# Kernel tuning notes

Hardware: AMD Instinct MI355X
Metric: run time of the kernel (lower is better)

The kernel has to match this reference:

```python
import jax, jax.numpy as jnp
import numpy as np

L, B, N, C = 6, 8, 300, 20
H, W = 28, 28
GT_H, GT_W = 448, 448


def _pair_similarity(rm_b):
    # rm_b: (N, H, W). Pairwise (IoU + Dice)/2 between thresholded (>0.7) masks.
    T = (rm_b.reshape(N, H * W) > 0.7).astype(jnp.float32)
    inter = T @ T.T                                  # (N, N)
    s = T.sum(axis=1)
    union = s[:, None] + s[None, :] - inter
    tot = s[:, None] + s[None, :]
    iou = jnp.where(union == 0, 1.0, inter / jnp.where(union == 0, 1.0, union))
    dice = jnp.where(tot == 0, 1.0, 2.0 * inter / jnp.where(tot == 0, 1.0, tot))
    return 0.5 * (iou + dice)


def _cluster(S_b, cls_sc):
    # NMS-style greedy transitive expansion from the top-scoring candidate.
    # Equivalent to the torch while-loop: fin_{k+1} = {j in cand : max_{i in fin_k} S[i,j] > 0.5}
    cand = cls_sc > 0.01
    has_cand = jnp.any(cand)
    adj = S_b > 0.5                                   # (N, N) similarity graph
    seed = jnp.argmax(jnp.where(cand, cls_sc, -jnp.inf))
    fin0 = cand & adj[seed]                           # seed always included (S[seed,seed]=1)

    def cond(st):
        return st[1]

    def body(st):
        fin = st[0]
        new = cand & jnp.any(adj & fin[:, None], axis=0)
        return (new, jnp.any(new != fin))

    fin = jax.lax.while_loop(cond, body, (fin0, jnp.array(True)))[0]
    fallback = jnp.arange(N) == jnp.argmax(cls_sc)    # no candidate above 0.01 -> argmax only
    return jnp.where(has_cand, fin, fallback)


def _safe_log(x):
    # matches torch BCELoss log clamping (log clamped at -100)
    return jnp.where(x > 0, jnp.log(jnp.maximum(x, 1e-38)), -100.0)


def _forward(score_map, score, label, gt):
    # per-query CAMs, relu'd and max-normalized
    rm = jax.nn.relu(jnp.mean(score_map, axis=0).reshape(B, N, H, W))
    mx = jnp.max(rm, axis=(-2, -1), keepdims=True)
    rm = rm / (mx + 1e-6)

    S = jax.lax.stop_gradient(jax.vmap(_pair_similarity)(rm))   # (B, N, N)
    sc = jax.lax.stop_gradient(score)                            # used only in comparisons

    def pair_loss(rm_b, S_b, sc_b, gt_b, c):
        fin = _cluster(S_b, sc_b[:, c]).astype(jnp.float32)      # (N,)
        # mean over selected masks commutes with bilinear resize (linear op)
        mean_map = jnp.einsum('n,nhw->hw', fin, rm_b) / jnp.sum(fin)
        pred = jax.image.resize(mean_map, (GT_H, GT_W), method='linear')  # align_corners=False
        y = (gt_b == c + 1).astype(jnp.float32)
        return -jnp.mean(y * _safe_log(pred) + (1.0 - y) * _safe_log(1.0 - pred))

    cls = jnp.arange(C)
    per_b = jax.vmap(lambda rm_b, S_b, sc_b, gt_b:
                     jax.vmap(lambda c: pair_loss(rm_b, S_b, sc_b, gt_b, c))(cls))
    losses = per_b(rm, S, sc, gt)                                # (B, C)
    act = (label != 0).astype(jnp.float32)
    return jnp.sum(losses * act) / jnp.sum(act)


def setup_inputs() -> dict:
    key = jax.random.key(0)
    k1, k2, k3, k4 = jax.random.split(key, 4)
    return {
        'score_map': jax.random.normal(k1, (L, B, N, H * W), dtype=jnp.float32),
        'score': jax.random.uniform(k2, (B, N, C), dtype=jnp.float32),
        'label': jax.random.randint(k3, (B, C), 0, 2).astype(jnp.int32),
        'gt': jax.random.randint(k4, (B, GT_H, GT_W), 0, C + 1).astype(jnp.int32),
    }


def reference(score_map, score, label, gt):
    return _forward(score_map, score, label, gt)
```

## Files before the change

### kernel.cpp

```cpp
#include <hip/hip_runtime.h>
#include <math.h>

#define LNUM 6
#define BNUM 8
#define NNUM 300
#define CNUM 20
#define HW   784
#define HW4  196
#define GH   448
#define NW   16
#define AW   5
#define RTILE 16
#define NTILE 28

__device__ float              g_rm [BNUM*NNUM*HW];
__device__ unsigned long long g_T  [BNUM*NNUM*NW];
__device__ int                g_s  [BNUM*NNUM];
__device__ unsigned long long g_adj[BNUM*NNUM*AW];
__device__ float              g_mm [BNUM*CNUM*HW];
__device__ double             g_part[BNUM*CNUM*NTILE];

__global__ void k_rm(const float* __restrict__ sm) {
    int bn  = blockIdx.x;
    int tid = threadIdx.x;
    int lane = tid & 63, wid = tid >> 6;
    __shared__ float wmax[4];
    __shared__ int   scount;
    if (tid == 0) scount = 0;
    const size_t lstr4 = (size_t)BNUM * NNUM * HW4;
    const float4* base = (const float4*)sm + (size_t)bn * HW4;
    bool act = tid < HW4;
    float4 v = {0.f, 0.f, 0.f, 0.f};
    if (act) {
        float4 a = {0.f, 0.f, 0.f, 0.f};
        #pragma unroll
        for (int l = 0; l < LNUM; ++l) {
            float4 x = base[(size_t)l * lstr4 + tid];
            a.x += x.x; a.y += x.y; a.z += x.z; a.w += x.w;
        }
        v.x = fmaxf(__fdiv_rn(a.x, 6.0f), 0.0f);
        v.y = fmaxf(__fdiv_rn(a.y, 6.0f), 0.0f);
        v.z = fmaxf(__fdiv_rn(a.z, 6.0f), 0.0f);
        v.w = fmaxf(__fdiv_rn(a.w, 6.0f), 0.0f);
    }
    float lm = fmaxf(fmaxf(v.x, v.y), fmaxf(v.z, v.w));
    #pragma unroll
    for (int off = 32; off; off >>= 1) lm = fmaxf(lm, __shfl_xor(lm, off));
    if (lane == 0) wmax[wid] = lm;
    __syncthreads();
    float mx = fmaxf(fmaxf(wmax[0], wmax[1]), fmaxf(wmax[2], wmax[3]));
    float d = mx + 1e-6f;
    float4 nv;
    nv.x = __fdiv_rn(v.x, d); nv.y = __fdiv_rn(v.y, d);
    nv.z = __fdiv_rn(v.z, d); nv.w = __fdiv_rn(v.w, d);
    if (act) ((float4*)g_rm)[(size_t)bn * HW4 + tid] = nv;
    float c[4] = {nv.x, nv.y, nv.z, nv.w};
    #pragma unroll
    for (int k = 0; k < 4; ++k) {
        bool pr = act && (c[k] > 0.7f);
        unsigned long long ball = __ballot(pr);
        if (lane == 0) {
            g_T[(size_t)bn * NW + k * 4 + wid] = ball;
            atomicAdd(&scount, __popcll(ball));
        }
    }
    __syncthreads();
    if (tid == 0) g_s[bn] = scount;
}

__global__ void k_adj() {
    int blk = blockIdx.x;
    int b = blk / NNUM;
    int tid = threadIdx.x;
    __shared__ unsigned long long Ti[NW];
    __shared__ int si_sh;
    if (tid < NW)  Ti[tid] = g_T[(size_t)blk * NW + tid];
    if (tid == NW) si_sh = g_s[blk];
    __syncthreads();
    bool a = false;
    int j = tid;
    if (j < NNUM) {
        const unsigned long long* Tj = &g_T[((size_t)b * NNUM + j) * NW];
        int inter = 0;
        #pragma unroll
        for (int w = 0; w < NW; ++w) inter += __popcll(Ti[w] & Tj[w]);
        int si = si_sh, sj = g_s[b * NNUM + j];
        int uni = si + sj - inter, tot = si + sj;
        float iou  = (uni == 0) ? 1.0f : __fdiv_rn((float)inter, (float)uni);
        float dice = (tot == 0) ? 1.0f : __fdiv_rn(2.0f * (float)inter, (float)tot);
        a = (0.5f * (iou + dice)) > 0.5f;
    }
    unsigned long long ball = __ballot(a);
    if ((tid & 63) == 0) g_adj[(size_t)blk * AW + (tid >> 6)] = ball;
}

__global__ void k_cm(const float* __restrict__ score, const int* __restrict__ label) {
    int blk = blockIdx.x;
    if (label[blk] == 0) return;
    int b = blk / CNUM, c = blk - b * CNUM;
    int tid = threadIdx.x;
    int lane = tid & 63, wid = tid >> 6;
    __shared__ unsigned long long adj_sh[NNUM][AW];
    __shared__ unsigned long long cand[AW], fin[AW], nwv[AW];
    __shared__ int sh_has, sh_go;
    __shared__ float sh_cf;
    for (int idx = tid; idx < NNUM * AW; idx += 256)
        ((unsigned long long*)adj_sh)[idx] = g_adj[(size_t)b * NNUM * AW + idx];
    if (wid == 0) {
        float bv = -INFINITY; int bi = NNUM;
        float bva = -INFINITY; int bia = NNUM;
        for (int k = 0; k < AW; ++k) {
            int j = k * 64 + lane;
            bool cb = false;
            if (j < NNUM) {
                float sc = score[((size_t)b * NNUM + j) * CNUM + c];
                if (sc > bva) { bva = sc; bia = j; }
                cb = sc > 0.01f;
                if (cb && sc > bv) { bv = sc; bi = j; }
            }
            unsigned long long ball = __ballot(cb);
            if (lane == 0) cand[k] = ball;
        }
        #pragma unroll
        for (int off = 1; off < 64; off <<= 1) {
            float ov = __shfl_xor(bv, off);  int oi = __shfl_xor(bi, off);
            if (ov > bv || (ov == bv && oi < bi)) { bv = ov; bi = oi; }
            float ova = __shfl_xor(bva, off); int oia = __shfl_xor(bia, off);
            if (ova > bva || (ova == bva && oia < bia)) { bva = ova; bia = oia; }
        }
        bool has = (cand[0] | cand[1] | cand[2] | cand[3] | cand[4]) != 0ULL;
        if (lane == 0) sh_has = has ? 1 : 0;
        if (has) {
            if (lane < AW) fin[lane] = cand[lane] & adj_sh[bi][lane];
        } else {
            if (lane < AW) fin[lane] = ((bia >> 6) == lane) ? (1ULL << (bia & 63)) : 0ULL;
        }
    }
    __syncthreads();
    if (sh_has) {
        for (int it = 0; it < NNUM + 2; ++it) {
            if (wid == 0) {
                for (int k = 0; k < AW; ++k) {
                    int j = k * 64 + lane;
                    bool nb = false;
                    if (j < NNUM && ((cand[k] >> lane) & 1ULL)) {
                        unsigned long long o = (adj_sh[j][0] & fin[0]) | (adj_sh[j][1] & fin[1]) |
                                               (adj_sh[j][2] & fin[2]) | (adj_sh[j][3] & fin[3]) |
                                               (adj_sh[j][4] & fin[4]);
                        nb = (o != 0ULL);
                    }
                    unsigned long long ball = __ballot(nb);
                    if (lane == 0) nwv[k] = ball;
                }
                bool ch = (lane < AW) && (nwv[lane] != fin[lane]);
                unsigned long long chb = __ballot(ch);
                if (lane == 0) sh_go = (chb != 0ULL) ? 1 : 0;
                if (lane < AW) fin[lane] = nwv[lane];
            }
            __syncthreads();
            int go = sh_go;
            __syncthreads();
            if (!go) break;
        }
    }
    if (tid == 0) {
        int cs = 0;
        for (int w = 0; w < AW; ++w) cs += __popcll(fin[w]);
        sh_cf = (float)cs;
    }
    __syncthreads();
    if (tid < HW4) {
        float4 a = {0.f, 0.f, 0.f, 0.f};
        for (int w = 0; w < AW; ++w) {
            unsigned long long word = fin[w];
            while (word) {
                int j = w * 64 + (__ffsll(word) - 1);
                word &= word - 1;
                float4 r = ((const float4*)g_rm)[((size_t)b * NNUM + j) * HW4 + tid];
                a.x += r.x; a.y += r.y; a.z += r.z; a.w += r.w;
            }
        }
        float cc = sh_cf;
        float4 o;
        o.x = __fdiv_rn(a.x, cc); o.y = __fdiv_rn(a.y, cc);
        o.z = __fdiv_rn(a.z, cc); o.w = __fdiv_rn(a.w, cc);
        ((float4*)g_mm)[(size_t)blk * HW4 + tid] = o;
    }
}

__global__ void k_bce(const int* __restrict__ gt, const int* __restrict__ label) {
    int blk = blockIdx.x;
    int bc = blk / NTILE, tile = blk - bc * NTILE;
    if (label[bc] == 0) return;
    int b = bc / CNUM, c = bc - b * CNUM;
    int tid = threadIdx.x;
    __shared__ float m[HW];
    __shared__ float rowY[RTILE * 28];
    __shared__ double wsum[7];
    if (tid < HW4) ((float4*)m)[tid] = ((const float4*)g_mm)[(size_t)bc * HW4 + tid];
    __syncthreads();
    int row0 = tile * RTILE;
    {
        int r = tid / 28, x = tid - r * 28;
        int oy = row0 + r;
        float iy = fmaf((float)oy, 0.0625f, -0.46875f);
        float y0f = floorf(iy);
        float wy = iy - y0f;
        int y0 = (int)y0f;
        if (y0 < 0) { y0 = 0; wy = 0.0f; } else if (y0 > 26) { y0 = 26; wy = 1.0f; }
        float lo = m[y0 * 28 + x], hi = m[y0 * 28 + 28 + x];
        rowY[tid] = lo + wy * (hi - lo);
    }
    __syncthreads();
    int r = tid / 28, j = tid - r * 28;
    const int* gr = gt + ((size_t)b * GH + row0 + r) * GH;
    double acc = 0.0;
    int cp1 = c + 1;
    if (j < 27) {
        float rY0 = rowY[r * 28 + j], rY1 = rowY[r * 28 + j + 1];
        float sl = rY1 - rY0;
        const int4* gp = (const int4*)(gr + 16 * j + 8);
        #pragma unroll
        for (int q = 0; q < 4; ++q) {
            int4 g4 = gp[q];
            #pragma unroll
            for (int u = 0; u < 4; ++u) {
                int k = q * 4 + u;
                int gv = (u == 0) ? g4.x : (u == 1) ? g4.y : (u == 2) ? g4.z : g4.w;
                float wk = fmaf((float)k, 0.0625f, 0.03125f);
                float pred = rY0 + wk * sl;
                float xv = (gv == cp1) ? pred : 1.0f - pred;
                float lg = __logf(fmaxf(xv, 1.175494351e-38f));
                acc += (double)((xv > 0.0f) ? lg : -100.0f);
            }
        }
    } else {
        #pragma unroll
        for (int side = 0; side < 2; ++side) {
            float pred = rowY[r * 28 + (side ? 27 : 0)];
            const int4* gp = (const int4*)(gr + (side ? 440 : 0));
            int4 a0 = gp[0], a1 = gp[1];
            int np = (a0.x == cp1) + (a0.y == cp1) + (a0.z == cp1) + (a0.w == cp1)
                   + (a1.x == cp1) + (a1.y == cp1) + (a1.z == cp1) + (a1.w == cp1);
            float om = 1.0f - pred;
            float lgp = (pred > 0.0f) ? __logf(fmaxf(pred, 1.175494351e-38f)) : -100.0f;
            float lgn = (om   > 0.0f) ? __logf(fmaxf(om,   1.175494351e-38f)) : -100.0f;
            acc += (double)lgp * (double)np + (double)lgn * (double)(8 - np);
        }
    }
    #pragma unroll
    for (int off = 32; off; off >>= 1) acc += __shfl_xor(acc, off);
    if ((tid & 63) == 0) wsum[tid >> 6] = acc;
    __syncthreads();
    if (tid == 0) {
        double s = 0.0;
        #pragma unroll
        for (int w = 0; w < 7; ++w) s += wsum[w];
        g_part[blk] = -s * (1.0 / (448.0 * 448.0));
    }
}

__global__ void k_final(const int* __restrict__ label, float* __restrict__ out) {
    int tid = threadIdx.x;
    double s = 0.0;
    for (int i = tid; i < BNUM * CNUM * NTILE; i += 256)
        if (label[i / NTILE] != 0) s += g_part[i];
    #pragma unroll
    for (int off = 32; off; off >>= 1) s += __shfl_xor(s, off);
    __shared__ double wsum[4];
    if ((tid & 63) == 0) wsum[tid >> 6] = s;
    __syncthreads();
    if (tid == 0) {
        int sa = 0;
        for (int i = 0; i < BNUM * CNUM; ++i) sa += (label[i] != 0) ? 1 : 0;
        out[0] = (float)((wsum[0] + wsum[1] + wsum[2] + wsum[3]) / (double)sa);
    }
}

extern "C" void kernel_launch(void* const* d_in, const int* in_sizes, int n_in,
                              void* d_out, int out_size, void* d_ws, size_t ws_size,
                              hipStream_t stream) {
    const float* sm    = (const float*)d_in[0];
    const float* score = (const float*)d_in[1];
    const int*   label = (const int*)d_in[2];
    const int*   gt    = (const int*)d_in[3];
    float* out = (float*)d_out;

    hipLaunchKernelGGL(k_rm,    dim3(BNUM * NNUM),         dim3(256), 0, stream, sm);
    hipLaunchKernelGGL(k_adj,   dim3(BNUM * NNUM),         dim3(320), 0, stream);
    hipLaunchKernelGGL(k_cm,    dim3(BNUM * CNUM),         dim3(256), 0, stream, score, label);
    hipLaunchKernelGGL(k_bce,   dim3(BNUM * CNUM * NTILE), dim3(448), 0, stream, gt, label);
    hipLaunchKernelGGL(k_final, dim3(1),                   dim3(256), 0, stream, label, out);
}
```

Measured before the change: 63.00 us.

## Fuse clustering, BCE and final reduction into one tiled kernel

Merges the clustering, BCE and final-reduction kernels into a single kernel launched per (batch, class, row-tile). Each tile block redoes the cluster expansion itself and builds only the three mean-map rows it needs, so the global mean-map buffer goes away. The final sum is done by the last block to finish, found through atomic counters, which removes two launches. The cost is 28x repeated clustering work, including adjacency loads into shared memory. The final sum also adds g_part entries for inactive labels unconditionally, which relies on those slots never having been written.

After: 189.8 us. +201.3%, slower.

```diff
diff --git a/kernel.cpp b/kernel.cpp
--- a/kernel.cpp
+++ b/kernel.cpp
@@ -10,15 +10,18 @@
 #define GH   448
 #define NW   16
 #define AW   5
-#define RTILE 16
+#define RT   16
 #define NTILE 28
+#define TOTBC  (BNUM*CNUM)
+#define TOTBLK (TOTBC*NTILE)
 
 __device__ float              g_rm [BNUM*NNUM*HW];
 __device__ unsigned long long g_T  [BNUM*NNUM*NW];
 __device__ int                g_s  [BNUM*NNUM];
 __device__ unsigned long long g_adj[BNUM*NNUM*AW];
-__device__ float              g_mm [BNUM*CNUM*HW];
-__device__ double             g_part[BNUM*CNUM*NTILE];
+__device__ double             g_part[TOTBLK];
+__device__ int                g_tdone[TOTBC];
+__device__ int                g_bdone = 0;
 
 __global__ void k_rm(const float* __restrict__ sm) {
     int bn  = blockIdx.x;
@@ -94,201 +97,215 @@
     if ((tid & 63) == 0) g_adj[(size_t)blk * AW + (tid >> 6)] = ball;
 }
 
-__global__ void k_cm(const float* __restrict__ score, const int* __restrict__ label) {
+__global__ void __launch_bounds__(448)
+k_bcf(const float* __restrict__ score, const int* __restrict__ label,
+      const int* __restrict__ gt, float* __restrict__ out) {
     int blk = blockIdx.x;
-    if (label[blk] == 0) return;
-    int b = blk / CNUM, c = blk - b * CNUM;
+    int bc = blk / NTILE, tile = blk - bc * NTILE;
+    int b = bc / CNUM, c = bc - b * CNUM;
     int tid = threadIdx.x;
     int lane = tid & 63, wid = tid >> 6;
+    bool active = (label[bc] != 0);
+
     __shared__ unsigned long long adj_sh[NNUM][AW];
     __shared__ unsigned long long cand[AW], fin[AW], nwv[AW];
-    __shared__ int sh_has, sh_go;
+    __shared__ int sh_has, sh_go, sh_last, sh_sa;
     __shared__ float sh_cf;
-    for (int idx = tid; idx < NNUM * AW; idx += 256)
-        ((unsigned long long*)adj_sh)[idx] = g_adj[(size_t)b * NNUM * AW + idx];
-    if (wid == 0) {
-        float bv = -INFINITY; int bi = NNUM;
-        float bva = -INFINITY; int bia = NNUM;
-        for (int k = 0; k < AW; ++k) {
-            int j = k * 64 + lane;
-            bool cb = false;
-            if (j < NNUM) {
-                float sc = score[((size_t)b * NNUM + j) * CNUM + c];
-                if (sc > bva) { bva = sc; bia = j; }
-                cb = sc > 0.01f;
-                if (cb && sc > bv) { bv = sc; bi = j; }
-            }
-            unsigned long long ball = __ballot(cb);
-            if (lane == 0) cand[k] = ball;
+    __shared__ float mrow[3 * 28];
+    __shared__ float rowY[RT * 28];
+    __shared__ double wsum[7];
+
+    if (active) {
+        for (int idx = tid; idx < NNUM * AW; idx += 448)
+            ((unsigned long long*)adj_sh)[idx] = g_adj[(size_t)b * NNUM * AW + idx];
+        if (wid == 0) {
+            float bv = -INFINITY; int bi = NNUM;
+            float bva = -INFINITY; int bia = NNUM;
+            for (int k = 0; k < AW; ++k) {
+                int j = k * 64 + lane;
+                bool cb = false;
+                if (j < NNUM) {
+                    float sc = score[((size_t)b * NNUM + j) * CNUM + c];
+                    if (sc > bva) { bva = sc; bia = j; }
+                    cb = sc > 0.01f;
+                    if (cb && sc > bv) { bv = sc; bi = j; }
+                }
+                unsigned long long ball = __ballot(cb);
+                if (lane == 0) cand[k] = ball;
+            }
+            #pragma unroll
+            for (int off = 1; off < 64; off <<= 1) {
+                float ov = __shfl_xor(bv, off);  int oi = __shfl_xor(bi, off);
+                if (ov > bv || (ov == bv && oi < bi)) { bv = ov; bi = oi; }
+                float ova = __shfl_xor(bva, off); int oia = __shfl_xor(bia, off);
+                if (ova > bva || (ova == bva && oia < bia)) { bva = ova; bia = oia; }
+            }
+            bool has = (cand[0] | cand[1] | cand[2] | cand[3] | cand[4]) != 0ULL;
+            if (lane == 0) sh_has = has ? 1 : 0;
+            if (has) {
+                if (lane < AW) fin[lane] = cand[lane] & adj_sh[bi][lane];
+            } else {
+                if (lane < AW) fin[lane] = ((bia >> 6) == lane) ? (1ULL << (bia & 63)) : 0ULL;
+            }
+        }
+        __syncthreads();
+        if (sh_has) {
+            for (int it = 0; it < NNUM + 2; ++it) {
+                if (wid == 0) {
+                    for (int k = 0; k < AW; ++k) {
+                        int j = k * 64 + lane;
+                        bool nb = false;
+                        if (j < NNUM && ((cand[k] >> lane) & 1ULL)) {
+                            unsigned long long o =
+                                (adj_sh[j][0] & fin[0]) | (adj_sh[j][1] & fin[1]) |
+                                (adj_sh[j][2] & fin[2]) | (adj_sh[j][3] & fin[3]) |
+                                (adj_sh[j][4] & fin[4]);
+                            nb = (o != 0ULL);
+                        }
+                        unsigned long long ball = __ballot(nb);
+                        if (lane == 0) nwv[k] = ball;
+                    }
+                    bool ch = (lane < AW) && (nwv[lane] != fin[lane]);
+                    unsigned long long chb = __ballot(ch);
+                    if (lane == 0) sh_go = (chb != 0ULL) ? 1 : 0;
+                    if (lane < AW) fin[lane] = nwv[lane];
+                }
+                __syncthreads();
+                int go = sh_go;
+                __syncthreads();
+                if (!go) break;
+            }
+        }
+        if (tid == 0) {
+            int cs = 0;
+            for (int w = 0; w < AW; ++w) cs += __popcll(fin[w]);
+            sh_cf = (float)cs;
+        }
+        __syncthreads();
+        int rlo = (tile > 0)  ? tile - 1 : 0;
+        int rhi = (tile < 27) ? tile + 1 : 27;
+        int nr = rhi - rlo + 1;
+        if (tid < nr * 28) {
+            int r = rlo + tid / 28, x = tid - (tid / 28) * 28;
+            float a = 0.f;
+            for (int w = 0; w < AW; ++w) {
+                unsigned long long word = fin[w];
+                while (word) {
+                    int j = w * 64 + (__ffsll(word) - 1);
+                    word &= word - 1;
+                    a += g_rm[((size_t)b * NNUM + j) * HW + r * 28 + x];
+                }
+            }
+            mrow[tid] = __fdiv_rn(a, sh_cf);
+        }
+        __syncthreads();
+        int row0 = tile * RT;
+        {
+            int r = tid / 28, x = tid - (tid / 28) * 28;
+            int oy = row0 + r;
+            float iy = fmaf((float)oy, 0.0625f, -0.46875f);
+            float y0f = floorf(iy);
+            float wy = iy - y0f;
+            int y0 = (int)y0f;
+            if (y0 < 0) { y0 = 0; wy = 0.0f; } else if (y0 > 26) { y0 = 26; wy = 1.0f; }
+            float lo = mrow[(y0 - rlo) * 28 + x], hi = mrow[(y0 - rlo + 1) * 28 + x];
+            rowY[tid] = lo + wy * (hi - lo);
+        }
+        __syncthreads();
+        double acc = 0.0;
+        {
+            int r = tid / 28, j = tid - (tid / 28) * 28;
+            const int* gr = gt + ((size_t)b * GH + row0 + r) * GH;
+            int cp1 = c + 1;
+            if (j < 27) {
+                float rY0 = rowY[r * 28 + j], rY1 = rowY[r * 28 + j + 1];
+                float sl = rY1 - rY0;
+                const int4* gp = (const int4*)(gr + 16 * j + 8);
+                #pragma unroll
+                for (int q = 0; q < 4; ++q) {
+                    int4 g4 = gp[q];
+                    #pragma unroll
+                    for (int uu = 0; uu < 4; ++uu) {
+                        int k = q * 4 + uu;
+                        int gv = (uu == 0) ? g4.x : (uu == 1) ? g4.y : (uu == 2) ? g4.z : g4.w;
+                        float wk = fmaf((float)k, 0.0625f, 0.03125f);
+                        float pred = rY0 + wk * sl;
+                        float xv = (gv == cp1) ? pred : 1.0f - pred;
+                        float lg = __logf(fmaxf(xv, 1.175494351e-38f));
+                        acc += (double)((xv > 0.0f) ? lg : -100.0f);
+                    }
+                }
+            } else {
+                #pragma unroll
+                for (int side = 0; side < 2; ++side) {
+                    float pred = rowY[r * 28 + (side ? 27 : 0)];
+                    const int4* gp = (const int4*)(gr + (side ? 440 : 0));
+                    int4 a0 = gp[0], a1 = gp[1];
+                    int np = (a0.x == cp1) + (a0.y == cp1) + (a0.z == cp1) + (a0.w == cp1)
+                           + (a1.x == cp1) + (a1.y == cp1) + (a1.z == cp1) + (a1.w == cp1);
+                    float om = 1.0f - pred;
+                    float lgp = (pred > 0.0f) ? __logf(fmaxf(pred, 1.175494351e-38f)) : -100.0f;
+                    float lgn = (om   > 0.0f) ? __logf(fmaxf(om,   1.175494351e-38f)) : -100.0f;
+                    acc += (double)lgp * (double)np + (double)lgn * (double)(8 - np);
+                }
+            }
         }
         #pragma unroll
-        for (int off = 1; off < 64; off <<= 1) {
-            float ov = __shfl_xor(bv, off);  int oi = __shfl_xor(bi, off);
-            if (ov > bv || (ov == bv && oi < bi)) { bv = ov; bi = oi; }
-            float ova = __shfl_xor(bva, off); int oia = __shfl_xor(bia, off);
-            if (ova > bva || (ova == bva && oia < bia)) { bva = ova; bia = oia; }
-        }
-        bool has = (cand[0] | cand[1] | cand[2] | cand[3] | cand[4]) != 0ULL;
-        if (lane == 0) sh_has = has ? 1 : 0;
-        if (has) {
-            if (lane < AW) fin[lane] = cand[lane] & adj_sh[bi][lane];
-        } else {
-            if (lane < AW) fin[lane] = ((bia >> 6) == lane) ? (1ULL << (bia & 63)) : 0ULL;
+        for (int off = 32; off; off >>= 1) acc += __shfl_xor(acc, off);
+        if (lane == 0) wsum[wid] = acc;
+        __syncthreads();
+        if (tid == 0) {
+            double s = 0.0;
+            #pragma unroll
+            for (int w = 0; w < 7; ++w) s += wsum[w];
+            g_part[blk] = -s * (1.0 / (448.0 * 448.0));
+        }
+    }
+
+    if (tid == 0) {
+        sh_last = 0;
+        __builtin_amdgcn_fence(__ATOMIC_RELEASE, "agent");
+        int t = __hip_atomic_fetch_add(&g_tdone[bc], 1, __ATOMIC_ACQ_REL, __HIP_MEMORY_SCOPE_AGENT);
+        if (t == NTILE - 1) {
+            __hip_atomic_store(&g_tdone[bc], 0, __ATOMIC_RELAXED, __HIP_MEMORY_SCOPE_AGENT);
+            int d = __hip_atomic_fetch_add(&g_bdone, 1, __ATOMIC_ACQ_REL, __HIP_MEMORY_SCOPE_AGENT);
+            if (d == TOTBC - 1) {
+                __hip_atomic_store(&g_bdone, 0, __ATOMIC_RELAXED, __HIP_MEMORY_SCOPE_AGENT);
+                sh_last = 1;
+            }
         }
     }
     __syncthreads();
-    if (sh_has) {
-        for (int it = 0; it < NNUM + 2; ++it) {
-            if (wid == 0) {
-                for (int k = 0; k < AW; ++k) {
-                    int j = k * 64 + lane;
-                    bool nb = false;
-                    if (j < NNUM && ((cand[k] >> lane) & 1ULL)) {
-                        unsigned long long o = (adj_sh[j][0] & fin[0]) | (adj_sh[j][1] & fin[1]) |
-                                               (adj_sh[j][2] & fin[2]) | (adj_sh[j][3] & fin[3]) |
-                                               (adj_sh[j][4] & fin[4]);
-                        nb = (o != 0ULL);
-                    }
-                    unsigned long long ball = __ballot(nb);
-                    if (lane == 0) nwv[k] = ball;
-                }
-                bool ch = (lane < AW) && (nwv[lane] != fin[lane]);
-                unsigned long long chb = __ballot(ch);
-                if (lane == 0) sh_go = (chb != 0ULL) ? 1 : 0;
-                if (lane < AW) fin[lane] = nwv[lane];
-            }
-            __syncthreads();
-            int go = sh_go;
-            __syncthreads();
-            if (!go) break;
-        }
-    }
-    if (tid == 0) {
-        int cs = 0;
-        for (int w = 0; w < AW; ++w) cs += __popcll(fin[w]);
-        sh_cf = (float)cs;
-    }
-    __syncthreads();
-    if (tid < HW4) {
-        float4 a = {0.f, 0.f, 0.f, 0.f};
-        for (int w = 0; w < AW; ++w) {
-            unsigned long long word = fin[w];
-            while (word) {
-                int j = w * 64 + (__ffsll(word) - 1);
-                word &= word - 1;
-                float4 r = ((const float4*)g_rm)[((size_t)b * NNUM + j) * HW4 + tid];
-                a.x += r.x; a.y += r.y; a.z += r.z; a.w += r.w;
-            }
-        }
-        float cc = sh_cf;
-        float4 o;
-        o.x = __fdiv_rn(a.x, cc); o.y = __fdiv_rn(a.y, cc);
-        o.z = __fdiv_rn(a.z, cc); o.w = __fdiv_rn(a.w, cc);
-        ((float4*)g_mm)[(size_t)blk * HW4 + tid] = o;
-    }
-}
-
-__global__ void k_bce(const int* __restrict__ gt, const int* __restrict__ label) {
-    int blk = blockIdx.x;
-    int bc = blk / NTILE, tile = blk - bc * NTILE;
-    if (label[bc] == 0) return;
-    int b = bc / CNUM, c = bc - b * CNUM;
-    int tid = threadIdx.x;
-    __shared__ float m[HW];
-    __shared__ float rowY[RTILE * 28];
-    __shared__ double wsum[7];
-    if (tid < HW4) ((float4*)m)[tid] = ((const float4*)g_mm)[(size_t)bc * HW4 + tid];
-    __syncthreads();
-    int row0 = tile * RTILE;
-    {
-        int r = tid / 28, x = tid - r * 28;
-        int oy = row0 + r;
-        float iy = fmaf((float)oy, 0.0625f, -0.46875f);
-        float y0f = floorf(iy);
-        float wy = iy - y0f;
-        int y0 = (int)y0f;
-        if (y0 < 0) { y0 = 0; wy = 0.0f; } else if (y0 > 26) { y0 = 26; wy = 1.0f; }
-        float lo = m[y0 * 28 + x], hi = m[y0 * 28 + 28 + x];
-        rowY[tid] = lo + wy * (hi - lo);
-    }
-    __syncthreads();
-    int r = tid / 28, j = tid - r * 28;
-    const int* gr = gt + ((size_t)b * GH + row0 + r) * GH;
-    double acc = 0.0;
-    int cp1 = c + 1;
-    if (j < 27) {
-        float rY0 = rowY[r * 28 + j], rY1 = rowY[r * 28 + j + 1];
-        float sl = rY1 - rY0;
-        const int4* gp = (const int4*)(gr + 16 * j + 8);
+    if (sh_last) {
+        __builtin_amdgcn_fence(__ATOMIC_ACQUIRE, "agent");
+        if (tid == 0) sh_sa = 0;
+        __syncthreads();
+        double s = 0.0;
+        for (int i = tid; i < TOTBLK; i += 448) s += g_part[i];
         #pragma unroll
-        for (int q = 0; q < 4; ++q) {
-            int4 g4 = gp[q];
+        for (int off = 32; off; off >>= 1) s += __shfl_xor(s, off);
+        if (lane == 0) wsum[wid] = s;
+        if (tid < TOTBC && label[tid] != 0) atomicAdd(&sh_sa, 1);
+        __syncthreads();
+        if (tid == 0) {
+            double tot = 0.0;
             #pragma unroll
-            for (int u = 0; u < 4; ++u) {
-                int k = q * 4 + u;
-                int gv = (u == 0) ? g4.x : (u == 1) ? g4.y : (u == 2) ? g4.z : g4.w;
-                float wk = fmaf((float)k, 0.0625f, 0.03125f);
-                float pred = rY0 + wk * sl;
-                float xv = (gv == cp1) ? pred : 1.0f - pred;
-                float lg = __logf(fmaxf(xv, 1.175494351e-38f));
-                acc += (double)((xv > 0.0f) ? lg : -100.0f);
-            }
-        }
-    } else {
-        #pragma unroll
-        for (int side = 0; side < 2; ++side) {
-            float pred = rowY[r * 28 + (side ? 27 : 0)];
-            const int4* gp = (const int4*)(gr + (side ? 440 : 0));
-            int4 a0 = gp[0], a1 = gp[1];
-            int np = (a0.x == cp1) + (a0.y == cp1) + (a0.z == cp1) + (a0.w == cp1)
-                   + (a1.x == cp1) + (a1.y == cp1) + (a1.z == cp1) + (a1.w == cp1);
-            float om = 1.0f - pred;
-            float lgp = (pred > 0.0f) ? __logf(fmaxf(pred, 1.175494351e-38f)) : -100.0f;
-            float lgn = (om   > 0.0f) ? __logf(fmaxf(om,   1.175494351e-38f)) : -100.0f;
-            acc += (double)lgp * (double)np + (double)lgn * (double)(8 - np);
-        }
-    }
-    #pragma unroll
-    for (int off = 32; off; off >>= 1) acc += __shfl_xor(acc, off);
-    if ((tid & 63) == 0) wsum[tid >> 6] = acc;
-    __syncthreads();
-    if (tid == 0) {
-        double s = 0.0;
-        #pragma unroll
-        for (int w = 0; w < 7; ++w) s += wsum[w];
-        g_part[blk] = -s * (1.0 / (448.0 * 448.0));
-    }
-}
-
-__global__ void k_final(const int* __restrict__ label, float* __restrict__ out) {
-    int tid = threadIdx.x;
-    double s = 0.0;
-    for (int i = tid; i < BNUM * CNUM * NTILE; i += 256)
-        if (label[i / NTILE] != 0) s += g_part[i];
-    #pragma unroll
-    for (int off = 32; off; off >>= 1) s += __shfl_xor(s, off);
-    __shared__ double wsum[4];
-    if ((tid & 63) == 0) wsum[tid >> 6] = s;
-    __syncthreads();
-    if (tid == 0) {
-        int sa = 0;
-        for (int i = 0; i < BNUM * CNUM; ++i) sa += (label[i] != 0) ? 1 : 0;
-        out[0] = (float)((wsum[0] + wsum[1] + wsum[2] + wsum[3]) / (double)sa);
+            for (int w = 0; w < 7; ++w) tot += wsum[w];
+            out[0] = (float)(tot / (double)sh_sa);
+        }
     }
 }
 
 extern "C" void kernel_launch(void* const* d_in, const int* in_sizes, int n_in,
                               void* d_out, int out_size, void* d_ws, size_t ws_size,
                               hipStream_t stream) {
-    const float* sm    = (const float*)d_in[0];
+    const float* smap  = (const float*)d_in[0];
     const float* score = (const float*)d_in[1];
     const int*   label = (const int*)d_in[2];
     const int*   gt    = (const int*)d_in[3];
     float* out = (float*)d_out;
 
-    hipLaunchKernelGGL(k_rm,    dim3(BNUM * NNUM),         dim3(256), 0, stream, sm);
-    hipLaunchKernelGGL(k_adj,   dim3(BNUM * NNUM),         dim3(320), 0, stream);
-    hipLaunchKernelGGL(k_cm,    dim3(BNUM * CNUM),         dim3(256), 0, stream, score, label);
-    hipLaunchKernelGGL(k_bce,   dim3(BNUM * CNUM * NTILE), dim3(448), 0, stream, gt, label);
-    hipLaunchKernelGGL(k_final, dim3(1),                   dim3(256), 0, stream, label, out);
+    hipLaunchKernelGGL(k_rm,  dim3(BNUM * NNUM), dim3(256), 0, stream, smap);
+    hipLaunchKernelGGL(k_adj, dim3(BNUM * NNUM), dim3(320), 0, stream);
+    hipLaunchKernelGGL(k_bcf, dim3(TOTBLK),      dim3(448), 0, stream, score, label, gt, out);
 }
```
